# Kernel optimization log

Measured on AMD Instinct MI355X. Metric: run time of the kernel, lower is better.

Reference implementation:

```python
import jax, jax.numpy as jnp
import numpy as np

H = 256        # hidden_dim
NH = 8         # num_heads
DH = H // NH   # head_dim
B, L1, L2 = 2, 512, 512


def setup_inputs() -> dict:
    key = jax.random.key(0)
    ks = jax.random.split(key, 8)
    s = 1.0 / np.sqrt(H)
    return {
        "embed1": jax.random.normal(ks[0], (B, L1, H), jnp.float32),
        "embed2": jax.random.normal(ks[1], (B, L2, H), jnp.float32),
        # nn.MultiheadAttention in-projection (packed q,k,v)
        "in_proj_w": jax.random.normal(ks[2], (3 * H, H), jnp.float32) * s,
        "in_proj_b": jax.random.normal(ks[3], (3 * H,), jnp.float32) * 0.01,
        # match_score MLP: Linear(2H -> H), Linear(H -> 1)
        "W1": jax.random.normal(ks[4], (H, 2 * H), jnp.float32) * (1.0 / np.sqrt(2 * H)),
        "b1": jax.random.normal(ks[5], (H,), jnp.float32) * 0.01,
        "W2": jax.random.normal(ks[6], (1, H), jnp.float32) * s,
        "b2": jax.random.normal(ks[7], (1,), jnp.float32) * 0.01,
    }


def reference(embed1, embed2, in_proj_w, in_proj_b, W1, b1, W2, b2):
    # ---- cross-attention weights (head-averaged, torch default) ----
    q = embed1 @ in_proj_w[:H].T + in_proj_b[:H]            # (B,L1,H)
    k = embed2 @ in_proj_w[H:2 * H].T + in_proj_b[H:2 * H]  # (B,L2,H)
    qh = q.reshape(B, L1, NH, DH)
    kh = k.reshape(B, L2, NH, DH)
    scale = 1.0 / np.sqrt(DH)
    logits = jnp.einsum('bqhd,bkhd->bhqk', qh, kh) * scale  # (B,NH,L1,L2)
    attn = jax.nn.softmax(logits, axis=-1)
    attn_weights = attn.mean(axis=1)                        # (B,L1,L2)

    # ---- pairwise MLP scorer: fused broadcast form of cat([e1,e2]) @ W1.T ----
    h1 = embed1 @ W1[:, :H].T                               # (B,L1,H)
    h2 = embed2 @ W1[:, H:].T                               # (B,L2,H)
    h = jax.nn.relu(h1[:, :, None, :] + h2[:, None, :, :] + b1)  # (B,L1,L2,H)
    match_scores = jax.nn.sigmoid(jnp.einsum('bijh,h->bij', h, W2[0]) + b2[0])
    return attn_weights, match_scores
```

## Files before the change

kernel.cpp:

```cpp
#include <hip/hip_runtime.h>
#include <hip/hip_bf16.h>
#include <stdint.h>

#define NHEADS 8
#define DHEAD 32
#define BB 2
#define LL 512
#define HH 256

__device__ __forceinline__ float bf_lo(unsigned u){ return __uint_as_float(u << 16); }
__device__ __forceinline__ float bf_hi(unsigned u){ return __uint_as_float(u & 0xffff0000u); }
__device__ __forceinline__ unsigned short f2bf(float f){
    unsigned u = __float_as_uint(f);
    u += 0x7fffu + ((u >> 16) & 1u);
    return (unsigned short)(u >> 16);
}
__device__ __forceinline__ void unpack8(uint4 u, float* f){
    f[0]=bf_lo(u.x); f[1]=bf_hi(u.x);
    f[2]=bf_lo(u.y); f[3]=bf_hi(u.y);
    f[4]=bf_lo(u.z); f[5]=bf_hi(u.z);
    f[6]=bf_lo(u.w); f[7]=bf_hi(u.w);
}

__global__ __launch_bounds__(256) void k_proj(
    const float* __restrict__ e1, const float* __restrict__ e2,
    const float* __restrict__ ipw, const float* __restrict__ ipb,
    const float* __restrict__ W1, const float* __restrict__ b1,
    unsigned short* __restrict__ wq, unsigned short* __restrict__ wk,
    unsigned short* __restrict__ wh1, unsigned short* __restrict__ wh2)
{
    __shared__ __align__(16) float es[8 * HH];
    const int t = threadIdx.x;
    const int g = blockIdx.x >> 7;
    const int row0 = (blockIdx.x & 127) << 3;
    const float* in = (g == 0 || g == 2) ? e1 : e2;
    {
        const float4* src = (const float4*)(in + (size_t)row0 * HH);
        float4* dst = (float4*)es;
        dst[t]       = src[t];
        dst[t + 256] = src[t + 256];
    }
    __syncthreads();
    const float* wrow; float bias = 0.f; float scale = 1.0f;
    if (g == 0)      { wrow = ipw + t * HH;            bias = ipb[t];      scale = 0.17677669529663689f; }
    else if (g == 1) { wrow = ipw + (HH + t) * HH;     bias = ipb[HH + t]; }
    else if (g == 2) { wrow = W1 + t * (2 * HH); }
    else             { wrow = W1 + t * (2 * HH) + HH;  bias = b1[t]; }

    float acc[8];
    #pragma unroll
    for (int r = 0; r < 8; r++) acc[r] = bias;
    #pragma unroll 4
    for (int kc = 0; kc < 64; kc++){
        float4 w4 = ((const float4*)wrow)[kc];
        #pragma unroll
        for (int r = 0; r < 8; r++){
            float4 e4 = ((const float4*)(es + r * HH))[kc];
            acc[r] = fmaf(e4.x, w4.x, fmaf(e4.y, w4.y, fmaf(e4.z, w4.z, fmaf(e4.w, w4.w, acc[r]))));
        }
    }
    unsigned short* outp = (g == 0) ? wq : ((g == 1) ? wk : ((g == 2) ? wh1 : wh2));
    #pragma unroll
    for (int r = 0; r < 8; r++)
        outp[(size_t)(row0 + r) * HH + t] = f2bf(acc[r] * scale);
}

__global__ __launch_bounds__(256) void k_logits(
    const unsigned short* __restrict__ wq, const unsigned short* __restrict__ wk,
    unsigned short* __restrict__ lg)
{
    __shared__ __align__(16) unsigned short Qs[64 * 40];
    __shared__ __align__(16) unsigned short Ks[64 * 40];
    const int t = threadIdx.x;
    const int blk = blockIdx.x;
    const int jt = blk & 7, it = (blk >> 3) & 7, h = (blk >> 6) & 7, b = blk >> 9;
    const int i0 = it * 64, j0 = jt * 64;
    {
        const int row = t >> 2, part = t & 3;
        const int sw = part ^ ((row >> 2) & 3);
        const uint4* qsrc = (const uint4*)(wq + ((size_t)(b * LL + i0 + row)) * HH + h * DHEAD);
        const uint4* ksrc = (const uint4*)(wk + ((size_t)(b * LL + j0 + row)) * HH + h * DHEAD);
        *(uint4*)(Qs + row * 40 + sw * 8) = qsrc[part];
        *(uint4*)(Ks + row * 40 + sw * 8) = ksrc[part];
    }
    __syncthreads();
    const int tx = t & 15, ty = t >> 4;
    float acc[4][4] = {};
    #pragma unroll
    for (int kc = 0; kc < 4; kc++){
        float qf[4][8], kf[4][8];
        #pragma unroll
        for (int r = 0; r < 4; r++){
            uint4 qu = *(const uint4*)(Qs + (ty * 4 + r) * 40 + (kc ^ (ty & 3)) * 8);
            unpack8(qu, qf[r]);
            uint4 ku = *(const uint4*)(Ks + (tx * 4 + r) * 40 + (kc ^ (tx & 3)) * 8);
            unpack8(ku, kf[r]);
        }
        #pragma unroll
        for (int ii = 0; ii < 4; ii++)
        #pragma unroll
        for (int jj = 0; jj < 4; jj++){
            float s = acc[ii][jj];
            #pragma unroll
            for (int e = 0; e < 8; e++) s = fmaf(qf[ii][e], kf[jj][e], s);
            acc[ii][jj] = s;
        }
    }
    #pragma unroll
    for (int ii = 0; ii < 4; ii++){
        const int i = i0 + ty * 4 + ii;
        ushort4 v;
        v.x = f2bf(acc[ii][0]); v.y = f2bf(acc[ii][1]);
        v.z = f2bf(acc[ii][2]); v.w = f2bf(acc[ii][3]);
        *(ushort4*)(lg + (((size_t)(b * LL + i) * NHEADS + h) << 9) + j0 + tx * 4) = v;
    }
}

__global__ __launch_bounds__(256) void k_softmax(
    const unsigned short* __restrict__ lg, float* __restrict__ outA)
{
    __shared__ float ms[8], invs[8];
    const int bi = blockIdx.x;
    const int t = threadIdx.x;
    const int h = t >> 5, g = t & 31;
    const uint4* src = (const uint4*)(lg + (size_t)bi * 4096 + h * 512 + g * 16);
    uint4 u0 = src[0], u1 = src[1];
    float v[16];
    unpack8(u0, v); unpack8(u1, v + 8);
    float m = v[0];
    #pragma unroll
    for (int e = 1; e < 16; e++) m = fmaxf(m, v[e]);
    #pragma unroll
    for (int mask = 1; mask < 32; mask <<= 1) m = fmaxf(m, __shfl_xor(m, mask, 64));
    float s = 0.f;
    #pragma unroll
    for (int e = 0; e < 16; e++) s += __expf(v[e] - m);
    #pragma unroll
    for (int mask = 1; mask < 32; mask <<= 1) s += __shfl_xor(s, mask, 64);
    if (g == 0){ ms[h] = m; invs[h] = 1.0f / (8.0f * s); }
    __syncthreads();
    float mm[8], ww[8];
    #pragma unroll
    for (int hh = 0; hh < 8; hh++){ mm[hh] = ms[hh]; ww[hh] = invs[hh]; }
    #pragma unroll
    for (int jj = 0; jj < 2; jj++){
        const int j = t + jj * 256;
        float o = 0.f;
        #pragma unroll
        for (int hh = 0; hh < 8; hh++){
            float lv = bf_lo((unsigned)lg[(size_t)bi * 4096 + hh * 512 + j]);
            o = fmaf(__expf(lv - mm[hh]), ww[hh], o);
        }
        outA[(size_t)bi * 512 + j] = o;
    }
}

__global__ __launch_bounds__(256) void k_match(
    const unsigned short* __restrict__ wh1, const unsigned short* __restrict__ wh2,
    const float* __restrict__ W2, const float* __restrict__ b2,
    float* __restrict__ outM)
{
    __shared__ __align__(16) unsigned short h1s[32 * 264];
    __shared__ __align__(16) unsigned short h2s[32 * 264];
    __shared__ __align__(16) float w2s[HH];
    const int t = threadIdx.x;
    const int blk = blockIdx.x;
    const int b = blk >> 8, it = (blk >> 4) & 15, jt = blk & 15;
    const int i0 = it * 32, j0 = jt * 32;
    w2s[t] = W2[t];
    {
        const uint4* s1 = (const uint4*)(wh1 + ((size_t)(b * LL + i0)) * HH);
        const uint4* s2 = (const uint4*)(wh2 + ((size_t)(b * LL + j0)) * HH);
        #pragma unroll
        for (int p = 0; p < 4; p++){
            const int idx = p * 256 + t;
            const int row = idx >> 5, col = idx & 31;
            ((uint4*)h1s)[row * 33 + col] = s1[idx];
            const int colw = col ^ ((row >> 1) & 7);
            ((uint4*)h2s)[row * 33 + colw] = s2[idx];
        }
    }
    __syncthreads();
    const int ti = t >> 4, tj = t & 15;
    const int sw = tj & 7;
    float a00 = 0.f, a01 = 0.f, a10 = 0.f, a11 = 0.f;
    #pragma unroll 4
    for (int hc = 0; hc < 32; hc++){
        uint4 ua = ((const uint4*)h1s)[(ti * 2    ) * 33 + hc];
        uint4 ub = ((const uint4*)h1s)[(ti * 2 + 1) * 33 + hc];
        uint4 uc = ((const uint4*)h2s)[(tj * 2    ) * 33 + (hc ^ sw)];
        uint4 ud = ((const uint4*)h2s)[(tj * 2 + 1) * 33 + (hc ^ sw)];
        float4 w0 = ((const float4*)w2s)[hc * 2];
        float4 w1 = ((const float4*)w2s)[hc * 2 + 1];
        float fa[8], fb[8], fc[8], fd[8];
        unpack8(ua, fa); unpack8(ub, fb); unpack8(uc, fc); unpack8(ud, fd);
        const float wv[8] = {w0.x, w0.y, w0.z, w0.w, w1.x, w1.y, w1.z, w1.w};
        #pragma unroll
        for (int e = 0; e < 8; e++){
            a00 = fmaf(fmaxf(fa[e] + fc[e], 0.f), wv[e], a00);
            a01 = fmaf(fmaxf(fa[e] + fd[e], 0.f), wv[e], a01);
            a10 = fmaf(fmaxf(fb[e] + fc[e], 0.f), wv[e], a10);
            a11 = fmaf(fmaxf(fb[e] + fd[e], 0.f), wv[e], a11);
        }
    }
    const float bb2 = b2[0];
    const int i = i0 + ti * 2, j = j0 + tj * 2;
    float* orow = outM + ((size_t)(b * LL + i)) * LL + j;
    float s00 = 1.f / (1.f + __expf(-(a00 + bb2)));
    float s01 = 1.f / (1.f + __expf(-(a01 + bb2)));
    float s10 = 1.f / (1.f + __expf(-(a10 + bb2)));
    float s11 = 1.f / (1.f + __expf(-(a11 + bb2)));
    *(float2*)orow        = make_float2(s00, s01);
    *(float2*)(orow + LL) = make_float2(s10, s11);
}

extern "C" void kernel_launch(void* const* d_in, const int* in_sizes, int n_in,
                              void* d_out, int out_size, void* d_ws, size_t ws_size,
                              hipStream_t stream)
{
    const float* e1  = (const float*)d_in[0];
    const float* e2  = (const float*)d_in[1];
    const float* ipw = (const float*)d_in[2];
    const float* ipb = (const float*)d_in[3];
    const float* W1  = (const float*)d_in[4];
    const float* b1  = (const float*)d_in[5];
    const float* W2  = (const float*)d_in[6];
    const float* b2  = (const float*)d_in[7];
    float* outA = (float*)d_out;
    float* outM = outA + (size_t)BB * LL * LL;

    unsigned short* ws  = (unsigned short*)d_ws;
    unsigned short* wq  = ws;
    unsigned short* wk  = ws + 262144;
    unsigned short* wh1 = ws + 524288;
    unsigned short* wh2 = ws + 786432;
    unsigned short* lg  = ws + 1048576;

    hipLaunchKernelGGL(k_proj,    dim3(512),  dim3(256), 0, stream,
                       e1, e2, ipw, ipb, W1, b1, wq, wk, wh1, wh2);
    hipLaunchKernelGGL(k_logits,  dim3(1024), dim3(256), 0, stream, wq, wk, lg);
    hipLaunchKernelGGL(k_softmax, dim3(1024), dim3(256), 0, stream, lg, outA);
    hipLaunchKernelGGL(k_match,   dim3(512),  dim3(256), 0, stream,
                       wh1, wh2, (const float*)W2, (const float*)b2, outM);
}
```

Baseline: 117.0 us.

## Rewrite pipeline with fp16 MFMA projections, fused attention, and packed-half match scorer

Switches intermediates from bf16 to fp16 and computes the projections with MFMA 16x16x32 instructions on swizzled shared-memory tiles. The separate logits and softmax kernels are replaced by one fused attention kernel that recomputes QK^T three times (max, sum, output) with MFMA and never writes logits to memory. The match scorer now does packed half add, relu and dot2 with larger per-thread tiles. Trade-offs: fp16 rounding changes accuracy, the attention kernel launches only 64 blocks so occupancy is low, and it does triple recompute.

```diff
diff --git a/kernel.cpp b/kernel.cpp
--- a/kernel.cpp
+++ b/kernel.cpp
@@ -1,217 +1,276 @@
 #include <hip/hip_runtime.h>
-#include <hip/hip_bf16.h>
+#include <hip/hip_fp16.h>
 #include <stdint.h>
 
-#define NHEADS 8
-#define DHEAD 32
-#define BB 2
+typedef _Float16 f16x8 __attribute__((ext_vector_type(8)));
+typedef _Float16 f16x2 __attribute__((ext_vector_type(2)));
+typedef float f32x4 __attribute__((ext_vector_type(4)));
+
 #define LL 512
 #define HH 256
 
-__device__ __forceinline__ float bf_lo(unsigned u){ return __uint_as_float(u << 16); }
-__device__ __forceinline__ float bf_hi(unsigned u){ return __uint_as_float(u & 0xffff0000u); }
-__device__ __forceinline__ unsigned short f2bf(float f){
-    unsigned u = __float_as_uint(f);
-    u += 0x7fffu + ((u >> 16) & 1u);
-    return (unsigned short)(u >> 16);
-}
-__device__ __forceinline__ void unpack8(uint4 u, float* f){
-    f[0]=bf_lo(u.x); f[1]=bf_hi(u.x);
-    f[2]=bf_lo(u.y); f[3]=bf_hi(u.y);
-    f[4]=bf_lo(u.z); f[5]=bf_hi(u.z);
-    f[6]=bf_lo(u.w); f[7]=bf_hi(u.w);
-}
+__device__ __forceinline__ unsigned pkrtz(float a, float b){
+    return __builtin_bit_cast(unsigned, __builtin_amdgcn_cvt_pkrtz(a, b));
+}
+
+#if __has_builtin(__builtin_amdgcn_fdot2)
+__device__ __forceinline__ float fdot2(f16x2 x, f16x2 w, float acc){
+    return __builtin_amdgcn_fdot2(x, w, acc, false);
+}
+#else
+__device__ __forceinline__ float fdot2(f16x2 x, f16x2 w, float acc){
+    return fmaf((float)x[0], (float)w[0], fmaf((float)x[1], (float)w[1], acc));
+}
+#endif
 
 __global__ __launch_bounds__(256) void k_proj(
     const float* __restrict__ e1, const float* __restrict__ e2,
     const float* __restrict__ ipw, const float* __restrict__ ipb,
     const float* __restrict__ W1, const float* __restrict__ b1,
-    unsigned short* __restrict__ wq, unsigned short* __restrict__ wk,
-    unsigned short* __restrict__ wh1, unsigned short* __restrict__ wh2)
+    _Float16* __restrict__ wq, _Float16* __restrict__ wk,
+    _Float16* __restrict__ wh1, _Float16* __restrict__ wh2)
 {
-    __shared__ __align__(16) float es[8 * HH];
-    const int t = threadIdx.x;
-    const int g = blockIdx.x >> 7;
-    const int row0 = (blockIdx.x & 127) << 3;
-    const float* in = (g == 0 || g == 2) ? e1 : e2;
-    {
-        const float4* src = (const float4*)(in + (size_t)row0 * HH);
-        float4* dst = (float4*)es;
-        dst[t]       = src[t];
-        dst[t + 256] = src[t + 256];
-    }
-    __syncthreads();
-    const float* wrow; float bias = 0.f; float scale = 1.0f;
-    if (g == 0)      { wrow = ipw + t * HH;            bias = ipb[t];      scale = 0.17677669529663689f; }
-    else if (g == 1) { wrow = ipw + (HH + t) * HH;     bias = ipb[HH + t]; }
-    else if (g == 2) { wrow = W1 + t * (2 * HH); }
-    else             { wrow = W1 + t * (2 * HH) + HH;  bias = b1[t]; }
-
-    float acc[8];
-    #pragma unroll
-    for (int r = 0; r < 8; r++) acc[r] = bias;
-    #pragma unroll 4
-    for (int kc = 0; kc < 64; kc++){
-        float4 w4 = ((const float4*)wrow)[kc];
-        #pragma unroll
-        for (int r = 0; r < 8; r++){
-            float4 e4 = ((const float4*)(es + r * HH))[kc];
-            acc[r] = fmaf(e4.x, w4.x, fmaf(e4.y, w4.y, fmaf(e4.z, w4.z, fmaf(e4.w, w4.w, acc[r]))));
-        }
-    }
-    unsigned short* outp = (g == 0) ? wq : ((g == 1) ? wk : ((g == 2) ? wh1 : wh2));
-    #pragma unroll
-    for (int r = 0; r < 8; r++)
-        outp[(size_t)(row0 + r) * HH + t] = f2bf(acc[r] * scale);
-}
-
-__global__ __launch_bounds__(256) void k_logits(
-    const unsigned short* __restrict__ wq, const unsigned short* __restrict__ wk,
-    unsigned short* __restrict__ lg)
-{
-    __shared__ __align__(16) unsigned short Qs[64 * 40];
-    __shared__ __align__(16) unsigned short Ks[64 * 40];
+    __shared__ __align__(16) _Float16 As[64 * 256];
+    __shared__ __align__(16) _Float16 Bs[64 * 256];
     const int t = threadIdx.x;
     const int blk = blockIdx.x;
-    const int jt = blk & 7, it = (blk >> 3) & 7, h = (blk >> 6) & 7, b = blk >> 9;
-    const int i0 = it * 64, j0 = jt * 64;
-    {
-        const int row = t >> 2, part = t & 3;
-        const int sw = part ^ ((row >> 2) & 3);
-        const uint4* qsrc = (const uint4*)(wq + ((size_t)(b * LL + i0 + row)) * HH + h * DHEAD);
-        const uint4* ksrc = (const uint4*)(wk + ((size_t)(b * LL + j0 + row)) * HH + h * DHEAD);
-        *(uint4*)(Qs + row * 40 + sw * 8) = qsrc[part];
-        *(uint4*)(Ks + row * 40 + sw * 8) = ksrc[part];
-    }
-    __syncthreads();
-    const int tx = t & 15, ty = t >> 4;
-    float acc[4][4] = {};
-    #pragma unroll
-    for (int kc = 0; kc < 4; kc++){
-        float qf[4][8], kf[4][8];
+    const int g = blk >> 6, mt = (blk >> 2) & 15, nt = blk & 3;
+    const int m0 = mt * 64, n0 = nt * 64;
+    const float* abase = (g == 0 || g == 2) ? e1 : e2;
+    const float* bbase; int bstride;
+    if (g == 0)      { bbase = ipw;         bstride = 256; }
+    else if (g == 1) { bbase = ipw + 65536; bstride = 256; }
+    else if (g == 2) { bbase = W1;          bstride = 512; }
+    else             { bbase = W1 + 256;    bstride = 512; }
+
+    #pragma unroll
+    for (int s = 0; s < 8; s++){
+        const int c = s * 256 + t;
+        const int row = c >> 5, kg = c & 31;
+        const int dst = row * 256 + ((kg ^ (row & 7)) << 3);
+        {
+            const float4* sa = (const float4*)(abase + (size_t)(m0 + row) * 256 + kg * 8);
+            float4 a0 = sa[0], a1 = sa[1];
+            uint4 pk = { pkrtz(a0.x, a0.y), pkrtz(a0.z, a0.w),
+                         pkrtz(a1.x, a1.y), pkrtz(a1.z, a1.w) };
+            *(uint4*)(As + dst) = pk;
+        }
+        {
+            const float4* sb = (const float4*)(bbase + (size_t)(n0 + row) * bstride + kg * 8);
+            float4 b0 = sb[0], b1v = sb[1];
+            uint4 pk = { pkrtz(b0.x, b0.y), pkrtz(b0.z, b0.w),
+                         pkrtz(b1v.x, b1v.y), pkrtz(b1v.z, b1v.w) };
+            *(uint4*)(Bs + dst) = pk;
+        }
+    }
+    __syncthreads();
+    const int w = t >> 6, l = t & 63;
+    const int lr = l & 15, lg = l >> 4;
+    f32x4 acc[4] = {};
+    const int brow = w * 16 + lr;
+    #pragma unroll
+    for (int kk = 0; kk < 8; kk++){
+        const int cb = ((kk * 4 + lg) ^ (lr & 7)) << 3;
+        f16x8 bf = *(const f16x8*)(Bs + brow * 256 + cb);
+        #pragma unroll
+        for (int ms = 0; ms < 4; ms++){
+            f16x8 af = *(const f16x8*)(As + (ms * 16 + lr) * 256 + cb);
+            acc[ms] = __builtin_amdgcn_mfma_f32_16x16x32_f16(af, bf, acc[ms], 0, 0, 0);
+        }
+    }
+    const int n = n0 + w * 16 + lr;
+    float bias = 0.f, scale = 1.f;
+    if (g == 0)      { bias = ipb[n];       scale = 0.17677669529663689f; }
+    else if (g == 1) { bias = ipb[256 + n]; }
+    else if (g == 3) { bias = b1[n]; }
+    _Float16* outp = (g == 0) ? wq : ((g == 1) ? wk : ((g == 2) ? wh1 : wh2));
+    #pragma unroll
+    for (int ms = 0; ms < 4; ms++)
         #pragma unroll
         for (int r = 0; r < 4; r++){
-            uint4 qu = *(const uint4*)(Qs + (ty * 4 + r) * 40 + (kc ^ (ty & 3)) * 8);
-            unpack8(qu, qf[r]);
-            uint4 ku = *(const uint4*)(Ks + (tx * 4 + r) * 40 + (kc ^ (tx & 3)) * 8);
-            unpack8(ku, kf[r]);
-        }
-        #pragma unroll
-        for (int ii = 0; ii < 4; ii++)
-        #pragma unroll
-        for (int jj = 0; jj < 4; jj++){
-            float s = acc[ii][jj];
-            #pragma unroll
-            for (int e = 0; e < 8; e++) s = fmaf(qf[ii][e], kf[jj][e], s);
-            acc[ii][jj] = s;
-        }
-    }
-    #pragma unroll
-    for (int ii = 0; ii < 4; ii++){
-        const int i = i0 + ty * 4 + ii;
-        ushort4 v;
-        v.x = f2bf(acc[ii][0]); v.y = f2bf(acc[ii][1]);
-        v.z = f2bf(acc[ii][2]); v.w = f2bf(acc[ii][3]);
-        *(ushort4*)(lg + (((size_t)(b * LL + i) * NHEADS + h) << 9) + j0 + tx * 4) = v;
-    }
-}
-
-__global__ __launch_bounds__(256) void k_softmax(
-    const unsigned short* __restrict__ lg, float* __restrict__ outA)
+            const int m = m0 + ms * 16 + lg * 4 + r;
+            outp[(size_t)m * 256 + n] = (_Float16)((acc[ms][r] + bias) * scale);
+        }
+}
+
+__global__ __launch_bounds__(256) void k_attn(
+    const _Float16* __restrict__ wq, const _Float16* __restrict__ wk,
+    float* __restrict__ outA)
 {
-    __shared__ float ms[8], invs[8];
-    const int bi = blockIdx.x;
+    __shared__ float sm[4][8][16];
+    __shared__ float fm[8][16];
+    __shared__ float fi[8][16];
     const int t = threadIdx.x;
-    const int h = t >> 5, g = t & 31;
-    const uint4* src = (const uint4*)(lg + (size_t)bi * 4096 + h * 512 + g * 16);
-    uint4 u0 = src[0], u1 = src[1];
-    float v[16];
-    unpack8(u0, v); unpack8(u1, v + 8);
-    float m = v[0];
-    #pragma unroll
-    for (int e = 1; e < 16; e++) m = fmaxf(m, v[e]);
-    #pragma unroll
-    for (int mask = 1; mask < 32; mask <<= 1) m = fmaxf(m, __shfl_xor(m, mask, 64));
-    float s = 0.f;
-    #pragma unroll
-    for (int e = 0; e < 16; e++) s += __expf(v[e] - m);
-    #pragma unroll
-    for (int mask = 1; mask < 32; mask <<= 1) s += __shfl_xor(s, mask, 64);
-    if (g == 0){ ms[h] = m; invs[h] = 1.0f / (8.0f * s); }
-    __syncthreads();
-    float mm[8], ww[8];
-    #pragma unroll
-    for (int hh = 0; hh < 8; hh++){ mm[hh] = ms[hh]; ww[hh] = invs[hh]; }
-    #pragma unroll
-    for (int jj = 0; jj < 2; jj++){
-        const int j = t + jj * 256;
-        float o = 0.f;
-        #pragma unroll
-        for (int hh = 0; hh < 8; hh++){
-            float lv = bf_lo((unsigned)lg[(size_t)bi * 4096 + hh * 512 + j]);
-            o = fmaf(__expf(lv - mm[hh]), ww[hh], o);
-        }
-        outA[(size_t)bi * 512 + j] = o;
+    const int b = blockIdx.x >> 5;
+    const int i0 = (blockIdx.x & 31) << 4;
+    const int w = t >> 6, l = t & 63, lr = l & 15, lg = l >> 4;
+
+    const _Float16* qrow = wq + (size_t)(b * LL + i0 + lr) * HH + lg * 8;
+    f16x8 q[8];
+    #pragma unroll
+    for (int h = 0; h < 8; h++) q[h] = *(const f16x8*)(qrow + h * 32);
+
+    const _Float16* kbase = wk + (size_t)(b * LL) * HH + lg * 8;
+    const f32x4 zero = {};
+    float m2[8][4];
+
+    #pragma unroll
+    for (int h = 0; h < 8; h++){
+        float m4[4] = {-3e38f, -3e38f, -3e38f, -3e38f};
+        for (int p = 0; p < 8; p++){
+            const int j0 = (p * 4 + w) << 4;
+            f16x8 kf = *(const f16x8*)(kbase + (size_t)(j0 + lr) * HH + h * 32);
+            f32x4 a = __builtin_amdgcn_mfma_f32_16x16x32_f16(q[h], kf, zero, 0, 0, 0);
+            #pragma unroll
+            for (int r = 0; r < 4; r++) m4[r] = fmaxf(m4[r], a[r]);
+        }
+        #pragma unroll
+        for (int r = 0; r < 4; r++){
+            #pragma unroll
+            for (int mask = 1; mask < 16; mask <<= 1)
+                m4[r] = fmaxf(m4[r], __shfl_xor(m4[r], mask, 64));
+        }
+        if (lr == 0){
+            #pragma unroll
+            for (int r = 0; r < 4; r++) sm[w][h][lg * 4 + r] = m4[r];
+        }
+    }
+    __syncthreads();
+    if (t < 128){
+        const int h = t >> 4, i = t & 15;
+        fm[h][i] = fmaxf(fmaxf(sm[0][h][i], sm[1][h][i]),
+                         fmaxf(sm[2][h][i], sm[3][h][i]));
+    }
+    __syncthreads();
+    #pragma unroll
+    for (int h = 0; h < 8; h++)
+        #pragma unroll
+        for (int r = 0; r < 4; r++) m2[h][r] = fm[h][lg * 4 + r];
+
+    #pragma unroll
+    for (int h = 0; h < 8; h++){
+        float s4[4] = {0.f, 0.f, 0.f, 0.f};
+        for (int p = 0; p < 8; p++){
+            const int j0 = (p * 4 + w) << 4;
+            f16x8 kf = *(const f16x8*)(kbase + (size_t)(j0 + lr) * HH + h * 32);
+            f32x4 a = __builtin_amdgcn_mfma_f32_16x16x32_f16(q[h], kf, zero, 0, 0, 0);
+            #pragma unroll
+            for (int r = 0; r < 4; r++) s4[r] += __expf(a[r] - m2[h][r]);
+        }
+        #pragma unroll
+        for (int r = 0; r < 4; r++){
+            #pragma unroll
+            for (int mask = 1; mask < 16; mask <<= 1)
+                s4[r] += __shfl_xor(s4[r], mask, 64);
+        }
+        if (lr == 0){
+            #pragma unroll
+            for (int r = 0; r < 4; r++) sm[w][h][lg * 4 + r] = s4[r];
+        }
+    }
+    __syncthreads();
+    if (t < 128){
+        const int h = t >> 4, i = t & 15;
+        fi[h][i] = 1.0f / (8.0f * (sm[0][h][i] + sm[1][h][i] + sm[2][h][i] + sm[3][h][i]));
+    }
+    __syncthreads();
+    float iv[8][4];
+    #pragma unroll
+    for (int h = 0; h < 8; h++)
+        #pragma unroll
+        for (int r = 0; r < 4; r++) iv[h][r] = fi[h][lg * 4 + r];
+
+    for (int p = 0; p < 8; p++){
+        const int j0 = (p * 4 + w) << 4;
+        f32x4 mean = {};
+        #pragma unroll
+        for (int h = 0; h < 8; h++){
+            f16x8 kf = *(const f16x8*)(kbase + (size_t)(j0 + lr) * HH + h * 32);
+            f32x4 a = __builtin_amdgcn_mfma_f32_16x16x32_f16(q[h], kf, zero, 0, 0, 0);
+            #pragma unroll
+            for (int r = 0; r < 4; r++) mean[r] += __expf(a[r] - m2[h][r]) * iv[h][r];
+        }
+        #pragma unroll
+        for (int r = 0; r < 4; r++)
+            outA[(size_t)(b * LL + i0 + lg * 4 + r) * LL + j0 + lr] = mean[r];
     }
 }
 
 __global__ __launch_bounds__(256) void k_match(
-    const unsigned short* __restrict__ wh1, const unsigned short* __restrict__ wh2,
+    const _Float16* __restrict__ wh1, const _Float16* __restrict__ wh2,
     const float* __restrict__ W2, const float* __restrict__ b2,
     float* __restrict__ outM)
 {
-    __shared__ __align__(16) unsigned short h1s[32 * 264];
-    __shared__ __align__(16) unsigned short h2s[32 * 264];
-    __shared__ __align__(16) float w2s[HH];
+    __shared__ __align__(16) _Float16 h1s[64 * 256];
+    __shared__ __align__(16) _Float16 h2s[32 * 256];
+    __shared__ __align__(16) f16x2 w2s[128];
     const int t = threadIdx.x;
     const int blk = blockIdx.x;
-    const int b = blk >> 8, it = (blk >> 4) & 15, jt = blk & 15;
-    const int i0 = it * 32, j0 = jt * 32;
-    w2s[t] = W2[t];
-    {
-        const uint4* s1 = (const uint4*)(wh1 + ((size_t)(b * LL + i0)) * HH);
-        const uint4* s2 = (const uint4*)(wh2 + ((size_t)(b * LL + j0)) * HH);
-        #pragma unroll
-        for (int p = 0; p < 4; p++){
-            const int idx = p * 256 + t;
-            const int row = idx >> 5, col = idx & 31;
-            ((uint4*)h1s)[row * 33 + col] = s1[idx];
-            const int colw = col ^ ((row >> 1) & 7);
-            ((uint4*)h2s)[row * 33 + colw] = s2[idx];
-        }
+    const int b = blk >> 7, it = (blk >> 4) & 7, jt = blk & 15;
+    const int i0 = it * 64, j0 = jt * 32;
+    if (t < 128){
+        unsigned pk = pkrtz(W2[2 * t], W2[2 * t + 1]);
+        w2s[t] = __builtin_bit_cast(f16x2, pk);
+    }
+    #pragma unroll
+    for (int s = 0; s < 8; s++){
+        const int c = s * 256 + t;
+        const int row = c >> 5, hc = c & 31;
+        uint4 v = *(const uint4*)(wh1 + (size_t)(b * LL + i0 + row) * HH + hc * 8);
+        *(uint4*)(h1s + row * 256 + ((hc ^ ((row >> 2) & 7)) << 3)) = v;
+    }
+    #pragma unroll
+    for (int s = 0; s < 4; s++){
+        const int c = s * 256 + t;
+        const int row = c >> 5, hc = c & 31;
+        uint4 v = *(const uint4*)(wh2 + (size_t)(b * LL + j0 + row) * HH + hc * 8);
+        *(uint4*)(h2s + row * 256 + ((hc ^ ((row >> 1) & 7)) << 3)) = v;
     }
     __syncthreads();
     const int ti = t >> 4, tj = t & 15;
-    const int sw = tj & 7;
-    float a00 = 0.f, a01 = 0.f, a10 = 0.f, a11 = 0.f;
-    #pragma unroll 4
+    float acc[4][2] = {};
     for (int hc = 0; hc < 32; hc++){
-        uint4 ua = ((const uint4*)h1s)[(ti * 2    ) * 33 + hc];
-        uint4 ub = ((const uint4*)h1s)[(ti * 2 + 1) * 33 + hc];
-        uint4 uc = ((const uint4*)h2s)[(tj * 2    ) * 33 + (hc ^ sw)];
-        uint4 ud = ((const uint4*)h2s)[(tj * 2 + 1) * 33 + (hc ^ sw)];
-        float4 w0 = ((const float4*)w2s)[hc * 2];
-        float4 w1 = ((const float4*)w2s)[hc * 2 + 1];
-        float fa[8], fb[8], fc[8], fd[8];
-        unpack8(ua, fa); unpack8(ub, fb); unpack8(uc, fc); unpack8(ud, fd);
-        const float wv[8] = {w0.x, w0.y, w0.z, w0.w, w1.x, w1.y, w1.z, w1.w};
-        #pragma unroll
-        for (int e = 0; e < 8; e++){
-            a00 = fmaf(fmaxf(fa[e] + fc[e], 0.f), wv[e], a00);
-            a01 = fmaf(fmaxf(fa[e] + fd[e], 0.f), wv[e], a01);
-            a10 = fmaf(fmaxf(fb[e] + fc[e], 0.f), wv[e], a10);
-            a11 = fmaf(fmaxf(fb[e] + fd[e], 0.f), wv[e], a11);
-        }
-    }
-    const float bb2 = b2[0];
-    const int i = i0 + ti * 2, j = j0 + tj * 2;
-    float* orow = outM + ((size_t)(b * LL + i)) * LL + j;
-    float s00 = 1.f / (1.f + __expf(-(a00 + bb2)));
-    float s01 = 1.f / (1.f + __expf(-(a01 + bb2)));
-    float s10 = 1.f / (1.f + __expf(-(a10 + bb2)));
-    float s11 = 1.f / (1.f + __expf(-(a11 + bb2)));
-    *(float2*)orow        = make_float2(s00, s01);
-    *(float2*)(orow + LL) = make_float2(s10, s11);
+        unsigned ua[4][4], uc[2][4], uw[4];
+        {
+            uint4 v;
+            #pragma unroll
+            for (int rr = 0; rr < 4; rr++){
+                v = *(const uint4*)(h1s + (ti * 4 + rr) * 256 + ((hc ^ (ti & 7)) << 3));
+                ua[rr][0] = v.x; ua[rr][1] = v.y; ua[rr][2] = v.z; ua[rr][3] = v.w;
+            }
+            #pragma unroll
+            for (int rr = 0; rr < 2; rr++){
+                v = *(const uint4*)(h2s + (tj * 2 + rr) * 256 + ((hc ^ (tj & 7)) << 3));
+                uc[rr][0] = v.x; uc[rr][1] = v.y; uc[rr][2] = v.z; uc[rr][3] = v.w;
+            }
+            v = *(const uint4*)(w2s + hc * 4);
+            uw[0] = v.x; uw[1] = v.y; uw[2] = v.z; uw[3] = v.w;
+        }
+        #pragma unroll
+        for (int e = 0; e < 4; e++){
+            const f16x2 wv = __builtin_bit_cast(f16x2, uw[e]);
+            #pragma unroll
+            for (int ii = 0; ii < 4; ii++){
+                const f16x2 av = __builtin_bit_cast(f16x2, ua[ii][e]);
+                #pragma unroll
+                for (int jj = 0; jj < 2; jj++){
+                    const f16x2 cv = __builtin_bit_cast(f16x2, uc[jj][e]);
+                    f16x2 x = av + cv;
+                    x = __builtin_elementwise_max(x, (f16x2)((_Float16)0.0f));
+                    acc[ii][jj] = fdot2(x, wv, acc[ii][jj]);
+                }
+            }
+        }
+    }
+    const float bb = b2[0];
+    #pragma unroll
+    for (int ii = 0; ii < 4; ii++){
+        const int i = i0 + ti * 4 + ii;
+        float2 o;
+        o.x = 1.0f / (1.0f + __expf(-(acc[ii][0] + bb)));
+        o.y = 1.0f / (1.0f + __expf(-(acc[ii][1] + bb)));
+        *(float2*)(outM + (size_t)(b * LL + i) * LL + j0 + tj * 2) = o;
+    }
 }
 
 extern "C" void kernel_launch(void* const* d_in, const int* in_sizes, int n_in,
@@ -227,19 +286,17 @@
     const float* W2  = (const float*)d_in[6];
     const float* b2  = (const float*)d_in[7];
     float* outA = (float*)d_out;
-    float* outM = outA + (size_t)BB * LL * LL;
-
-    unsigned short* ws  = (unsigned short*)d_ws;
-    unsigned short* wq  = ws;
-    unsigned short* wk  = ws + 262144;
-    unsigned short* wh1 = ws + 524288;
-    unsigned short* wh2 = ws + 786432;
-    unsigned short* lg  = ws + 1048576;
-
-    hipLaunchKernelGGL(k_proj,    dim3(512),  dim3(256), 0, stream,
+    float* outM = outA + (size_t)2 * LL * LL;
+
+    _Float16* ws  = (_Float16*)d_ws;
+    _Float16* wq  = ws;
+    _Float16* wk  = ws + 262144;
+    _Float16* wh1 = ws + 524288;
+    _Float16* wh2 = ws + 786432;
+
+    hipLaunchKernelGGL(k_proj,  dim3(256), dim3(256), 0, stream,
                        e1, e2, ipw, ipb, W1, b1, wq, wk, wh1, wh2);
-    hipLaunchKernelGGL(k_logits,  dim3(1024), dim3(256), 0, stream, wq, wk, lg);
-    hipLaunchKernelGGL(k_softmax, dim3(1024), dim3(256), 0, stream, lg, outA);
-    hipLaunchKernelGGL(k_match,   dim3(512),  dim3(256), 0, stream,
-                       wh1, wh2, (const float*)W2, (const float*)b2, outM);
-}
+    hipLaunchKernelGGL(k_attn,  dim3(64),  dim3(256), 0, stream, wq, wk, outA);
+    hipLaunchKernelGGL(k_match, dim3(256), dim3(256), 0, stream,
+                       wh1, wh2, W2, b2, outM);
+}
```

After: 111.4 us. -4.8%, faster.
